# Optimization experiments

Hardware: AMD Instinct MI355X
Metric: run time of the kernel (lower is better)

## Reference

```python
import jax, jax.numpy as jnp
import numpy as np

EPS = 1e-8  # torch CosineSimilarity eps
TEMP = 0.05

def _l2norm(x):
    n = jnp.sqrt(jnp.sum(x * x, axis=-1, keepdims=True))
    return x / jnp.maximum(n, EPS)

def setup_inputs() -> dict:
    key = jax.random.key(0)
    k1, k2, k3 = jax.random.split(key, 3)
    query = jax.random.normal(k1, (256, 768), dtype=jnp.float32)
    keys = jax.random.normal(k2, (256, 768), dtype=jnp.float32)
    queue = jax.random.normal(k3, (64, 1024, 768), dtype=jnp.float32)
    return {"query": query, "keys": keys, "queue": queue}

def reference(query, keys, queue):
    B, D = query.shape
    qn = _l2norm(query)                       # [B, D]
    kn = _l2norm(keys)                        # [B, D]
    negn = _l2norm(queue.reshape(-1, D))      # [N, D]
    sim_pos = jnp.einsum('bd,cd->bc', qn, kn)   # [B, B]
    sim_neg = jnp.einsum('bd,nd->bn', qn, negn) # [B, N]
    logits = jnp.concatenate([sim_pos, sim_neg], axis=1) / TEMP  # [B, B+N]
    target = jnp.arange(B)
    logp = jax.nn.log_softmax(logits, axis=-1)
    loss = -jnp.mean(logp[jnp.arange(B), target])
    return loss
```

## Files before the change

### kernel.cpp

```cpp
#include <hip/hip_runtime.h>
#include <hip/hip_bf16.h>

typedef __attribute__((ext_vector_type(8))) short short8;
typedef __attribute__((ext_vector_type(4))) float f32x4;

#define TEMP_INV 20.0f
#define NCH 1024

__device__ inline unsigned short f2bf(float f){
    unsigned int u = __builtin_bit_cast(unsigned int, f);
    u += 0x7fffu + ((u >> 16) & 1u);
    return (unsigned short)(u >> 16);
}
__device__ inline float bf2f(unsigned short h){
    unsigned int u = ((unsigned int)h) << 16;
    return __builtin_bit_cast(float, u);
}
__device__ inline unsigned int pk2bf(float a, float b){
    return (unsigned int)f2bf(a) | ((unsigned int)f2bf(b) << 16);
}

#define GLOAD16(src, dst) __builtin_amdgcn_global_load_lds( \
    (const __attribute__((address_space(1))) unsigned int*)(src), \
    (__attribute__((address_space(3))) unsigned int*)(dst), 16, 0, 0)

__global__ __launch_bounds__(256) void k_norm(const float* __restrict__ q,
                                              unsigned short* __restrict__ Aswz,
                                              float* __restrict__ out){
    int b = blockIdx.x, t = threadIdx.x;
    if (b == 0 && t == 0) out[0] = 0.f;
    const float* qr = q + b * 768;
    float v0 = qr[t], v1 = qr[t + 256], v2 = qr[t + 512];
    float ss = v0*v0 + v1*v1 + v2*v2;
#pragma unroll
    for (int o = 32; o; o >>= 1) ss += __shfl_xor(ss, o);
    __shared__ float red[4];
    if ((t & 63) == 0) red[t >> 6] = ss;
    __syncthreads();
    ss = red[0] + red[1] + red[2] + red[3];
    float inv = 1.0f / fmaxf(sqrtf(ss), 1e-8f);
    float nv[3] = {v0 * inv, v1 * inv, v2 * inv};
#pragma unroll
    for (int j = 0; j < 3; j++){
        int cc = t + 256 * j;
        unsigned short h = f2bf(nv[j]);
        int kc = cc >> 6, kl = cc & 63, g = kl >> 3, e = kl & 7;
        int slot = g ^ (b & 7);
        Aswz[kc * 16384 + b * 64 + slot * 8 + e] = h;
    }
}

__global__ __launch_bounds__(512, 4) void k_main(
        const float* __restrict__ keys,
        const float* __restrict__ queue,
        const unsigned short* __restrict__ Aswz,
        float* __restrict__ pmax,
        float* __restrict__ psum,
        float* __restrict__ diag){
    __shared__ unsigned short Atile[16384];
    __shared__ unsigned short Btile[4096];
    __shared__ unsigned short bxn16[768];
    __shared__ float invn[64];
    __shared__ float redm[2][256];
    __shared__ float reds[2][256];
    __shared__ float xred[2][256];
    __shared__ float wred[8];
    __shared__ float sxs;

    const int b = blockIdx.x, t = threadIdx.x;
    const int lane = t & 63;
    const int w = t >> 6;
    const int wm = w >> 1, wn = w & 1;
    const int frow = lane & 15, fg = lane >> 4;
    const int r = t >> 3, q8 = t & 7;
    const bool keyblk = (b < 256);

    if (keyblk){
        const float* krow = keys + b * 768;
        float v0 = krow[t];
        float v1 = (t < 256) ? krow[512 + t] : 0.f;
        float ssx = v0 * v0 + v1 * v1;
#pragma unroll
        for (int o = 32; o; o >>= 1) ssx += __shfl_xor(ssx, o);
        if (lane == 0) wred[w] = ssx;
        __syncthreads();
        if (t == 0){
            float s = 0.f;
#pragma unroll
            for (int i = 0; i < 8; i++) s += wred[i];
            sxs = 1.0f / fmaxf(sqrtf(s), 1e-8f);
        }
        __syncthreads();
        bxn16[t] = f2bf(v0 * sxs);
        if (t < 256) bxn16[512 + t] = f2bf(v1 * sxs);
        __syncthreads();
    }

    const float* rp = queue + (size_t)(b * 64 + r) * 768 + q8 * 4;
    const int xrow = t & 255, xk = t >> 8;

    float ssq = 0.f, dx = 0.f;
    f32x4 acc[4][2];
#pragma unroll
    for (int i = 0; i < 4; i++)
#pragma unroll
        for (int j = 0; j < 2; j++) acc[i][j] = (f32x4)0.f;

    for (int kc = 0; kc < 12; ++kc){
        if (kc) __syncthreads();
#pragma unroll
        for (int i = 0; i < 4; i++)
            GLOAD16(Aswz + kc * 16384 + i * 4096 + t * 8,
                    Atile + i * 4096 + t * 8);
        float4 u0 = *(const float4*)(rp + kc * 64);
        float4 u1 = *(const float4*)(rp + kc * 64 + 32);
        ssq += u0.x*u0.x + u0.y*u0.y + u0.z*u0.z + u0.w*u0.w;
        ssq += u1.x*u1.x + u1.y*u1.y + u1.z*u1.z + u1.w*u1.w;
        {
            int slot0 = (q8 >> 1) ^ (r & 7);
            int slot1 = ((q8 + 8) >> 1) ^ (r & 7);
            uint2 pk0, pk1;
            pk0.x = pk2bf(u0.x, u0.y); pk0.y = pk2bf(u0.z, u0.w);
            pk1.x = pk2bf(u1.x, u1.y); pk1.y = pk2bf(u1.z, u1.w);
            *(uint2*)&Btile[r * 64 + slot0 * 8 + (q8 & 1) * 4] = pk0;
            *(uint2*)&Btile[r * 64 + slot1 * 8 + (q8 & 1) * 4] = pk1;
        }
        __syncthreads();

#pragma unroll
        for (int ks = 0; ks < 2; ++ks){
            short8 af[4], bfv[2];
#pragma unroll
            for (int fm = 0; fm < 4; ++fm){
                int row = wm * 64 + fm * 16 + frow;
                int slot = (ks * 4 + fg) ^ (frow & 7);
                af[fm] = *(const short8*)&Atile[row * 64 + slot * 8];
            }
#pragma unroll
            for (int fn = 0; fn < 2; ++fn){
                int row = wn * 32 + fn * 16 + frow;
                int slot = (ks * 4 + fg) ^ (frow & 7);
                bfv[fn] = *(const short8*)&Btile[row * 64 + slot * 8];
            }
#pragma unroll
            for (int fm = 0; fm < 4; ++fm)
#pragma unroll
                for (int fn = 0; fn < 2; ++fn)
                    acc[fm][fn] = __builtin_amdgcn_mfma_f32_16x16x32_bf16(
                        af[fm], bfv[fn], acc[fm][fn], 0, 0, 0);
        }

        if (keyblk){
#pragma unroll
            for (int gi = 0; gi < 4; ++gi){
                int g = xk * 4 + gi;
                short8 av = *(const short8*)&Atile[xrow * 64 + (g ^ (xrow & 7)) * 8];
                short8 xv = *(const short8*)&bxn16[kc * 64 + g * 8];
#pragma unroll
                for (int e = 0; e < 8; ++e)
                    dx += bf2f((unsigned short)av[e]) * bf2f((unsigned short)xv[e]);
            }
        }
    }

    ssq += __shfl_xor(ssq, 1);
    ssq += __shfl_xor(ssq, 2);
    ssq += __shfl_xor(ssq, 4);
    if (q8 == 0) invn[r] = 1.0f / fmaxf(sqrtf(ssq), 1e-8f);
    if (keyblk) xred[xk][xrow] = dx;
    __syncthreads();

#pragma unroll
    for (int fm = 0; fm < 4; ++fm){
#pragma unroll
        for (int rr = 0; rr < 4; ++rr){
            float v0 = acc[fm][0][rr] * invn[wn * 32 + frow] * TEMP_INV;
            float v1 = acc[fm][1][rr] * invn[wn * 32 + 16 + frow] * TEMP_INV;
            int row = wm * 64 + fm * 16 + fg * 4 + rr;
            float m = fmaxf(v0, v1);
#pragma unroll
            for (int o = 1; o < 16; o <<= 1) m = fmaxf(m, __shfl_xor(m, o));
            float s = __expf(v0 - m) + __expf(v1 - m);
#pragma unroll
            for (int o = 1; o < 16; o <<= 1) s += __shfl_xor(s, o);
            if (frow == 0){ redm[wn][row] = m; reds[wn][row] = s; }
        }
    }
    __syncthreads();
    if (t < 256){
        float m0 = redm[0][t], m1 = redm[1][t];
        float M = fmaxf(m0, m1);
        float S = reds[0][t] * __expf(m0 - M) + reds[1][t] * __expf(m1 - M);
        if (keyblk){
            float vx = (xred[0][t] + xred[1][t]) * TEMP_INV;
            if (t == b) diag[b] = vx;
            float M2 = fmaxf(M, vx);
            S = S * __expf(M - M2) + __expf(vx - M2);
            M = M2;
        }
        pmax[b * 256 + t] = M;
        psum[b * 256 + t] = S;
    }
}

__global__ __launch_bounds__(256) void k_lse(const float* __restrict__ pmax,
                                             const float* __restrict__ psum,
                                             const float* __restrict__ diag,
                                             float* __restrict__ out){
    int b = blockIdx.x, t = threadIdx.x;
    float m = -1e30f;
    for (int cc = t; cc < NCH; cc += 256) m = fmaxf(m, pmax[cc * 256 + b]);
#pragma unroll
    for (int o = 32; o; o >>= 1) m = fmaxf(m, __shfl_xor(m, o));
    __shared__ float red[4];
    __shared__ float Msh;
    if ((t & 63) == 0) red[t >> 6] = m;
    __syncthreads();
    if (t == 0) Msh = fmaxf(fmaxf(red[0], red[1]), fmaxf(red[2], red[3]));
    __syncthreads();
    float M = Msh;
    float s = 0.f;
    for (int cc = t; cc < NCH; cc += 256) s += psum[cc * 256 + b] * __expf(pmax[cc * 256 + b] - M);
#pragma unroll
    for (int o = 32; o; o >>= 1) s += __shfl_xor(s, o);
    if ((t & 63) == 0) red[t >> 6] = s;
    __syncthreads();
    if (t == 0)
        atomicAdd(out, (M + logf(red[0] + red[1] + red[2] + red[3]) - diag[b]) * (1.0f / 256.0f));
}

extern "C" void kernel_launch(void* const* d_in, const int* in_sizes, int n_in,
                              void* d_out, int out_size, void* d_ws, size_t ws_size,
                              hipStream_t stream){
    const float* q  = (const float*)d_in[0];
    const float* k  = (const float*)d_in[1];
    const float* qu = (const float*)d_in[2];
    char* ws = (char*)d_ws;
    unsigned short* Aswz = (unsigned short*)(ws);
    float* diag  = (float*)(ws + 393216);
    float* pmax  = (float*)(ws + 394240);
    float* psum  = (float*)(ws + 1442816);

    k_norm<<<256, 256, 0, stream>>>(q, Aswz, (float*)d_out);
    k_main<<<1024, 512, 0, stream>>>(k, qu, Aswz, pmax, psum, diag);
    k_lse<<<256, 256, 0, stream>>>(pmax, psum, diag, (float*)d_out);
}
```

Before: 78.49 us.

## Widen main kernel tiles to 256 negatives per block with 1024 threads

Each block of the main kernel now handles 256 queue rows instead of 64, using 16 waves with a 4x4 MFMA fragment grid per wave. The grid shrinks from 1024 to 256 blocks, so every block is also a key block. The shared A tile of normalized queries is now reused across four times as many negatives, which cuts repeated A loads from L2 and the number of partial LSE entries. In exchange there are only 256 blocks on a 256-CU part, which may leave little occupancy to hide latency. The larger LDS footprint and register use per block could also limit concurrency.

Measured after the change: 77.87 us. No clear change (-0.8%).

```diff
diff --git a/kernel.cpp b/kernel.cpp
--- a/kernel.cpp
+++ b/kernel.cpp
@@ -5,7 +5,7 @@
 typedef __attribute__((ext_vector_type(4))) float f32x4;
 
 #define TEMP_INV 20.0f
-#define NCH 1024
+#define NCH 256
 
 __device__ inline unsigned short f2bf(float f){
     unsigned int u = __builtin_bit_cast(unsigned int, f);
@@ -50,7 +50,7 @@
     }
 }
 
-__global__ __launch_bounds__(512, 4) void k_main(
+__global__ __launch_bounds__(1024) void k_main(
         const float* __restrict__ keys,
         const float* __restrict__ queue,
         const unsigned short* __restrict__ Aswz,
@@ -58,28 +58,26 @@
         float* __restrict__ psum,
         float* __restrict__ diag){
     __shared__ unsigned short Atile[16384];
-    __shared__ unsigned short Btile[4096];
+    __shared__ unsigned short Btile[16384];
     __shared__ unsigned short bxn16[768];
-    __shared__ float invn[64];
-    __shared__ float redm[2][256];
-    __shared__ float reds[2][256];
-    __shared__ float xred[2][256];
-    __shared__ float wred[8];
+    __shared__ float invn[256];
+    __shared__ float redm[4][256];
+    __shared__ float reds[4][256];
+    __shared__ float xred[4][256];
+    __shared__ float wred[16];
     __shared__ float sxs;
 
     const int b = blockIdx.x, t = threadIdx.x;
     const int lane = t & 63;
     const int w = t >> 6;
-    const int wm = w >> 1, wn = w & 1;
+    const int wm = w >> 2, wn = w & 3;
     const int frow = lane & 15, fg = lane >> 4;
-    const int r = t >> 3, q8 = t & 7;
-    const bool keyblk = (b < 256);
-
-    if (keyblk){
-        const float* krow = keys + b * 768;
-        float v0 = krow[t];
-        float v1 = (t < 256) ? krow[512 + t] : 0.f;
-        float ssx = v0 * v0 + v1 * v1;
+    const int c = t >> 2, q4 = t & 3;
+    const int c7 = c & 7;
+
+    {
+        float v = (t < 768) ? keys[b * 768 + t] : 0.f;
+        float ssx = v * v;
 #pragma unroll
         for (int o = 32; o; o >>= 1) ssx += __shfl_xor(ssx, o);
         if (lane == 0) wred[w] = ssx;
@@ -87,100 +85,97 @@
         if (t == 0){
             float s = 0.f;
 #pragma unroll
-            for (int i = 0; i < 8; i++) s += wred[i];
+            for (int i = 0; i < 16; i++) s += wred[i];
             sxs = 1.0f / fmaxf(sqrtf(s), 1e-8f);
         }
         __syncthreads();
-        bxn16[t] = f2bf(v0 * sxs);
-        if (t < 256) bxn16[512 + t] = f2bf(v1 * sxs);
-        __syncthreads();
-    }
-
-    const float* rp = queue + (size_t)(b * 64 + r) * 768 + q8 * 4;
+        if (t < 768) bxn16[t] = f2bf(v * sxs);
+        __syncthreads();
+    }
+
+    const float* rp = queue + (size_t)(b * 256 + c) * 768 + q4 * 16;
     const int xrow = t & 255, xk = t >> 8;
 
     float ssq = 0.f, dx = 0.f;
-    f32x4 acc[4][2];
+    f32x4 acc[4][4];
 #pragma unroll
     for (int i = 0; i < 4; i++)
 #pragma unroll
-        for (int j = 0; j < 2; j++) acc[i][j] = (f32x4)0.f;
+        for (int j = 0; j < 4; j++) acc[i][j] = (f32x4)0.f;
 
     for (int kc = 0; kc < 12; ++kc){
         if (kc) __syncthreads();
-#pragma unroll
-        for (int i = 0; i < 4; i++)
-            GLOAD16(Aswz + kc * 16384 + i * 4096 + t * 8,
-                    Atile + i * 4096 + t * 8);
-        float4 u0 = *(const float4*)(rp + kc * 64);
-        float4 u1 = *(const float4*)(rp + kc * 64 + 32);
-        ssq += u0.x*u0.x + u0.y*u0.y + u0.z*u0.z + u0.w*u0.w;
-        ssq += u1.x*u1.x + u1.y*u1.y + u1.z*u1.z + u1.w*u1.w;
+        GLOAD16(Aswz + kc * 16384 + t * 8, Atile + t * 8);
+        GLOAD16(Aswz + kc * 16384 + 8192 + t * 8, Atile + 8192 + t * 8);
         {
-            int slot0 = (q8 >> 1) ^ (r & 7);
-            int slot1 = ((q8 + 8) >> 1) ^ (r & 7);
-            uint2 pk0, pk1;
+            float4 u0 = *(const float4*)(rp + kc * 64);
+            float4 u1 = *(const float4*)(rp + kc * 64 + 4);
+            float4 u2 = *(const float4*)(rp + kc * 64 + 8);
+            float4 u3 = *(const float4*)(rp + kc * 64 + 12);
+            ssq += u0.x*u0.x + u0.y*u0.y + u0.z*u0.z + u0.w*u0.w;
+            ssq += u1.x*u1.x + u1.y*u1.y + u1.z*u1.z + u1.w*u1.w;
+            ssq += u2.x*u2.x + u2.y*u2.y + u2.z*u2.z + u2.w*u2.w;
+            ssq += u3.x*u3.x + u3.y*u3.y + u3.z*u3.z + u3.w*u3.w;
+            uint4 pk0, pk1;
             pk0.x = pk2bf(u0.x, u0.y); pk0.y = pk2bf(u0.z, u0.w);
-            pk1.x = pk2bf(u1.x, u1.y); pk1.y = pk2bf(u1.z, u1.w);
-            *(uint2*)&Btile[r * 64 + slot0 * 8 + (q8 & 1) * 4] = pk0;
-            *(uint2*)&Btile[r * 64 + slot1 * 8 + (q8 & 1) * 4] = pk1;
+            pk0.z = pk2bf(u1.x, u1.y); pk0.w = pk2bf(u1.z, u1.w);
+            pk1.x = pk2bf(u2.x, u2.y); pk1.y = pk2bf(u2.z, u2.w);
+            pk1.z = pk2bf(u3.x, u3.y); pk1.w = pk2bf(u3.z, u3.w);
+            int slot0 = (q4 * 2) ^ c7;
+            int slot1 = (q4 * 2 + 1) ^ c7;
+            *(uint4*)&Btile[c * 64 + slot0 * 8] = pk0;
+            *(uint4*)&Btile[c * 64 + slot1 * 8] = pk1;
         }
         __syncthreads();
 
 #pragma unroll
         for (int ks = 0; ks < 2; ++ks){
-            short8 af[4], bfv[2];
-#pragma unroll
-            for (int fm = 0; fm < 4; ++fm){
-                int row = wm * 64 + fm * 16 + frow;
-                int slot = (ks * 4 + fg) ^ (frow & 7);
-                af[fm] = *(const short8*)&Atile[row * 64 + slot * 8];
-            }
-#pragma unroll
-            for (int fn = 0; fn < 2; ++fn){
-                int row = wn * 32 + fn * 16 + frow;
-                int slot = (ks * 4 + fg) ^ (frow & 7);
-                bfv[fn] = *(const short8*)&Btile[row * 64 + slot * 8];
-            }
+            const int slotv = (ks * 4 + fg) ^ (frow & 7);
+            short8 af[4], bfv[4];
 #pragma unroll
             for (int fm = 0; fm < 4; ++fm)
-#pragma unroll
-                for (int fn = 0; fn < 2; ++fn)
+                af[fm] = *(const short8*)&Atile[(wm * 64 + fm * 16 + frow) * 64 + slotv * 8];
+#pragma unroll
+            for (int fn = 0; fn < 4; ++fn)
+                bfv[fn] = *(const short8*)&Btile[(wn * 64 + fn * 16 + frow) * 64 + slotv * 8];
+#pragma unroll
+            for (int fm = 0; fm < 4; ++fm)
+#pragma unroll
+                for (int fn = 0; fn < 4; ++fn)
                     acc[fm][fn] = __builtin_amdgcn_mfma_f32_16x16x32_bf16(
                         af[fm], bfv[fn], acc[fm][fn], 0, 0, 0);
         }
 
-        if (keyblk){
-#pragma unroll
-            for (int gi = 0; gi < 4; ++gi){
-                int g = xk * 4 + gi;
-                short8 av = *(const short8*)&Atile[xrow * 64 + (g ^ (xrow & 7)) * 8];
-                short8 xv = *(const short8*)&bxn16[kc * 64 + g * 8];
-#pragma unroll
-                for (int e = 0; e < 8; ++e)
-                    dx += bf2f((unsigned short)av[e]) * bf2f((unsigned short)xv[e]);
-            }
+#pragma unroll
+        for (int gi = 0; gi < 2; ++gi){
+            int g = xk * 2 + gi;
+            short8 av = *(const short8*)&Atile[xrow * 64 + (g ^ (xrow & 7)) * 8];
+            short8 xv = *(const short8*)&bxn16[kc * 64 + g * 8];
+#pragma unroll
+            for (int e = 0; e < 8; ++e)
+                dx += bf2f((unsigned short)av[e]) * bf2f((unsigned short)xv[e]);
         }
     }
 
     ssq += __shfl_xor(ssq, 1);
     ssq += __shfl_xor(ssq, 2);
-    ssq += __shfl_xor(ssq, 4);
-    if (q8 == 0) invn[r] = 1.0f / fmaxf(sqrtf(ssq), 1e-8f);
-    if (keyblk) xred[xk][xrow] = dx;
+    if (q4 == 0) invn[c] = 1.0f / fmaxf(sqrtf(ssq), 1e-8f);
+    xred[xk][xrow] = dx;
     __syncthreads();
 
 #pragma unroll
     for (int fm = 0; fm < 4; ++fm){
 #pragma unroll
         for (int rr = 0; rr < 4; ++rr){
-            float v0 = acc[fm][0][rr] * invn[wn * 32 + frow] * TEMP_INV;
-            float v1 = acc[fm][1][rr] * invn[wn * 32 + 16 + frow] * TEMP_INV;
+            float v[4];
+#pragma unroll
+            for (int fn = 0; fn < 4; ++fn)
+                v[fn] = acc[fm][fn][rr] * invn[wn * 64 + fn * 16 + frow] * TEMP_INV;
             int row = wm * 64 + fm * 16 + fg * 4 + rr;
-            float m = fmaxf(v0, v1);
+            float m = fmaxf(fmaxf(v[0], v[1]), fmaxf(v[2], v[3]));
 #pragma unroll
             for (int o = 1; o < 16; o <<= 1) m = fmaxf(m, __shfl_xor(m, o));
-            float s = __expf(v0 - m) + __expf(v1 - m);
+            float s = __expf(v[0]-m) + __expf(v[1]-m) + __expf(v[2]-m) + __expf(v[3]-m);
 #pragma unroll
             for (int o = 1; o < 16; o <<= 1) s += __shfl_xor(s, o);
             if (frow == 0){ redm[wn][row] = m; reds[wn][row] = s; }
@@ -188,17 +183,19 @@
     }
     __syncthreads();
     if (t < 256){
-        float m0 = redm[0][t], m1 = redm[1][t];
-        float M = fmaxf(m0, m1);
-        float S = reds[0][t] * __expf(m0 - M) + reds[1][t] * __expf(m1 - M);
-        if (keyblk){
-            float vx = (xred[0][t] + xred[1][t]) * TEMP_INV;
-            if (t == b) diag[b] = vx;
-            float M2 = fmaxf(M, vx);
-            S = S * __expf(M - M2) + __expf(vx - M2);
-            M = M2;
-        }
-        pmax[b * 256 + t] = M;
+        float M = -1e30f, S = 0.f;
+#pragma unroll
+        for (int ww = 0; ww < 4; ++ww){
+            float m2 = redm[ww][t], s2 = reds[ww][t];
+            float Mn = fmaxf(M, m2);
+            S = S * __expf(M - Mn) + s2 * __expf(m2 - Mn);
+            M = Mn;
+        }
+        float vx = (xred[0][t] + xred[1][t] + xred[2][t] + xred[3][t]) * TEMP_INV;
+        if (t == b) diag[b] = vx;
+        float Mn = fmaxf(M, vx);
+        S = S * __expf(M - Mn) + __expf(vx - Mn);
+        pmax[b * 256 + t] = Mn;
         psum[b * 256 + t] = S;
     }
 }
@@ -239,9 +236,9 @@
     unsigned short* Aswz = (unsigned short*)(ws);
     float* diag  = (float*)(ws + 393216);
     float* pmax  = (float*)(ws + 394240);
-    float* psum  = (float*)(ws + 1442816);
+    float* psum  = (float*)(ws + 656384);
 
     k_norm<<<256, 256, 0, stream>>>(q, Aswz, (float*)d_out);
-    k_main<<<1024, 512, 0, stream>>>(k, qu, Aswz, pmax, psum, diag);
+    k_main<<<256, 1024, 0, stream>>>(k, qu, Aswz, pmax, psum, diag);
     k_lse<<<256, 256, 0, stream>>>(pmax, psum, diag, (float*)d_out);
 }
```
